# Kernel tuning notes

Measured on AMD Instinct MI355X. Metric: run time of the kernel, lower is better.

Reference implementation:

```python
import jax, jax.numpy as jnp
import numpy as np

SPATIAL_DIM = 2
N_IN = 4096
N_OUT = 1024
C_IN = 32
C_OUT = 32
FILTER_SEQ = (64, 64)
BATCH = 16


def _grid(num_points):
    # replicates: meshgrid(indexing='xy') of linspace(0,1,n) per dim, dstack, view(-1, d)
    n = int(num_points ** (1.0 / SPATIAL_DIM))
    nodes = np.linspace(0.0, 1.0, n)
    X, Y = np.meshgrid(nodes, nodes, indexing='xy')
    return np.dstack((X, Y)).reshape(-1, SPATIAL_DIM)  # (n^2, 2)


def _cache():
    # replicates QuadConvLayer.cache(): bump-support sparsity pattern
    out_locs = _grid(N_OUT)               # (N_OUT, 2)
    in_nodes = _grid(N_IN)                # (N_IN, 2)
    locs = out_locs[:, None, :] - in_nodes[None, :, :]   # (N_OUT, N_IN, 2)
    bump_arg = np.linalg.norm(locs, axis=2) ** 4
    decay_param = (N_IN / 16.0) ** 2
    mask = bump_arg <= 1.0 / decay_param
    idx = np.argwhere(mask)               # (E, 2), row-major sorted like torch.nonzero
    eval_locs = locs[mask]                # (E, 2)
    return eval_locs.astype(np.float32), idx.astype(np.int64)


def setup_inputs() -> dict:
    key = jax.random.key(0)
    k_feat, k1, k2, k3 = jax.random.split(key, 4)
    eval_locs, eval_indices = _cache()
    # filter MLP G: Linear(2,64,bias=False) -> Sin -> Linear(64,64) -> Sin -> Linear(64, C_IN*C_OUT)
    d0, d1, d2, d3 = SPATIAL_DIM, FILTER_SEQ[0], FILTER_SEQ[1], C_IN * C_OUT
    W1 = jax.random.normal(k1, (d0, d1), jnp.float32) / np.sqrt(d0)
    W2 = jax.random.normal(k2, (d1, d2), jnp.float32) / np.sqrt(d1)
    W3 = jax.random.normal(k3, (d2, d3), jnp.float32) / np.sqrt(d2)
    features = jax.random.normal(k_feat, (BATCH, C_IN, N_IN), jnp.float32)
    return {
        "features": features,
        "W1": W1,
        "W2": W2,
        "W3": W3,
        "eval_locs": jnp.asarray(eval_locs),
        "eval_indices": jnp.asarray(eval_indices),
    }


def reference(features, W1, W2, W3, eval_locs, eval_indices):
    B = features.shape[0]
    E = eval_locs.shape[0]
    seg = eval_indices[:, 0]   # output point per edge (sorted)
    src = eval_indices[:, 1]   # input point per edge
    # filter MLP with Sin activations: (E, 2) -> (E, C_IN, C_OUT)
    h = jnp.sin(eval_locs @ W1)
    h = jnp.sin(h @ W2)
    filt = (h @ W3).reshape(E, C_IN, C_OUT)
    # gather features at source points: (B, C_IN, E)
    gathered = features[:, :, src]
    # faithful to torch: a raw reshape (NOT a transpose) of (B, C_IN, E) -> (B, E, C_IN)
    g = gathered.reshape(B, E, C_IN)
    vals = jnp.einsum('bni,nij->bnj', g, filt)   # (B, E, C_OUT)
    # faithful raw reshape (B, E, C_OUT) -> (B, C_OUT, E)
    vals = vals.reshape(B, C_OUT, E)
    # scatter-sum over edges into output points (segment_coo sum)
    integral = jnp.zeros((B, C_OUT, N_OUT), features.dtype).at[:, :, seg].add(vals)
    return integral
```

## Files before the change

### kernel.cpp

```cpp
#include <hip/hip_runtime.h>
#include <hip/hip_bf16.h>

typedef __bf16 bf16x4  __attribute__((ext_vector_type(4)));
typedef __bf16 bf16x8  __attribute__((ext_vector_type(8)));
typedef __bf16 bf16x16 __attribute__((ext_vector_type(16)));
typedef float  f32x4   __attribute__((ext_vector_type(4)));

#define N_IN   4096
#define N_OUT  1024
#define BATCH  16
#define ROWS   16

#define H1_STR   72
#define H2_STR   72
#define FT_JSTR  40
#define FTH_NSTR 648
#define G_STR    520
#define V_STR    520
#define GSTR2    1048
#define VSTR2    1288
#define FB_FT_NSTR 1288
#define SEG_STR  34

#define WS_W3T_OFF    0
#define WS_W2T_OFF    131072
#define WS_FEATT_OFF  139264
#define WS_NEED       4333568

__global__ void qc_zero_kernel(float* __restrict__ out, int n4) {
    int i = blockIdx.x * blockDim.x + threadIdx.x;
    if (i < n4) ((float4*)out)[i] = make_float4(0.f, 0.f, 0.f, 0.f);
}

__global__ void qc_prep_kernel(const float* __restrict__ w3, const float* __restrict__ w2,
                               __bf16* __restrict__ w3t, __bf16* __restrict__ w2t) {
    int gid = blockIdx.x * blockDim.x + threadIdx.x;
    if (gid < 65536) {
        int k = gid & 63, col = gid >> 6;
        w3t[gid] = (__bf16)w3[k * 1024 + col];
    } else {
        int j = gid - 65536;
        int k = j & 63, col = j >> 6;
        w2t[j] = (__bf16)w2[k * 64 + col];
    }
}

__global__ void qc_prep2_kernel(const float* __restrict__ w3, const float* __restrict__ w2,
                                const float* __restrict__ feat,
                                float* __restrict__ out,
                                __bf16* __restrict__ w3t, __bf16* __restrict__ w2t,
                                __bf16* __restrict__ featT) {
    int bid = blockIdx.x, tid = threadIdx.x;
    if (bid < 512) {
        int c    = bid >> 4;
        int src  = (bid & 15) * 256 + tid;
        bf16x16 v;
        #pragma unroll
        for (int b = 0; b < 16; ++b)
            v[b] = (__bf16)feat[(b * 32 + c) * N_IN + src];
        __bf16* p = &featT[((size_t)c * N_IN + src) * 16];
        *(bf16x8*)p       = *(bf16x8*)&v;
        *(bf16x8*)(p + 8) = *((bf16x8*)&v + 1);
    } else if (bid < 528) {
        __shared__ float tile[64][65];
        const int colbase = (bid - 512) * 64;
        #pragma unroll
        for (int it = 0; it < 16; ++it) {
            int k = it * 4 + (tid >> 6);
            int c = tid & 63;
            tile[k][c] = w3[k * 1024 + colbase + c];
        }
        __syncthreads();
        int cc = tid >> 2;
        int k0 = (tid & 3) * 16;
        bf16x8 o0, o1;
        #pragma unroll
        for (int z = 0; z < 8; ++z) {
            o0[z] = (__bf16)tile[k0 + z][cc];
            o1[z] = (__bf16)tile[k0 + 8 + z][cc];
        }
        __bf16* wp = &w3t[(colbase + cc) * 64 + k0];
        *(bf16x8*)wp       = o0;
        *(bf16x8*)(wp + 8) = o1;
    } else if (bid == 528) {
        #pragma unroll
        for (int z = 0; z < 16; ++z) {
            int j = tid * 16 + z;
            w2t[j] = (__bf16)w2[(j & 63) * 64 + (j >> 6)];
        }
    } else {
        int i = (bid - 529) * 256 + tid;
        ((float4*)out)[i] = make_float4(0.f, 0.f, 0.f, 0.f);
    }
}

__global__ __launch_bounds__(512, 2)
void qc_fused32_kernel(const __bf16* __restrict__ featT,
                       const float* __restrict__ w1,
                       const float* __restrict__ locs,
                       const int*   __restrict__ eidx,
                       const __bf16* __restrict__ w2t,
                       const __bf16* __restrict__ w3t,
                       float* __restrict__ out,
                       int E)
{
    __shared__ __align__(16) unsigned char region1[41472];
    __shared__ __align__(16) __bf16 h1b[32 * H1_STR];
    __shared__ __align__(16) __bf16 h2b[32 * H2_STR];
    __shared__ unsigned short seg_s[32 * SEG_STR];

    __bf16* gb   = (__bf16*)region1;
    __bf16* ftv  = (__bf16*)region1;
    __bf16* vals = (__bf16*)region1;

    const int tid  = threadIdx.x;
    const int lane = tid & 63;
    const int wv   = tid >> 6;
    const int ml   = lane & 15;
    const int q    = lane >> 4;
    const int n0   = blockIdx.x * 32;
    const int t0   = n0 * 32;
    const int ch0  = t0 / E;
    const int m0   = t0 - ch0 * E;

    const int tlb = wv * 128 + lane;
    bf16x16 gvv[2];
    int sgv[2];
    #pragma unroll
    for (int h = 0; h < 2; ++h) {
        int tl = tlb + h * 64;
        int mm = m0 + tl;
        int cc = ch0 + (mm >= E);
        if (mm >= E) mm -= E;
        int2 p = ((const int2*)eidx)[mm];
        sgv[h] = p.x;
        int ccc = cc < 32 ? cc : 31;
        bf16x16 g = *(const bf16x16*)&featT[((size_t)ccc * N_IN + p.y) * 16];
        if (cc >= 32) {
            #pragma unroll
            for (int z = 0; z < 16; ++z) g[z] = (__bf16)0.f;
        }
        gvv[h] = g;
    }
    const int rg = (wv >> 2) * 16;
    const int cw = (wv & 3) * 16;
    const bf16x8 bw0 = *(const bf16x8*)&w2t[(cw + ml) * 64 + q * 8];
    const bf16x8 bw1 = *(const bf16x8*)&w2t[(cw + ml) * 64 + 32 + q * 8];

    {
        const int r  = tid >> 4;
        const int j0 = (tid & 15) * 4;
        float lx = 0.f, ly = 0.f;
        int n = n0 + r;
        if (n < E) { lx = locs[n * 2]; ly = locs[n * 2 + 1]; }
        float4 wa = *(const float4*)&w1[j0];
        float4 wb = *(const float4*)&w1[64 + j0];
        __bf16* hp = &h1b[r * H1_STR + j0];
        hp[0] = (__bf16)__sinf(lx * wa.x + ly * wb.x);
        hp[1] = (__bf16)__sinf(lx * wa.y + ly * wb.y);
        hp[2] = (__bf16)__sinf(lx * wa.z + ly * wb.z);
        hp[3] = (__bf16)__sinf(lx * wa.w + ly * wb.w);
    }
    __syncthreads();

    {
        bf16x8 a0 = *(const bf16x8*)&h1b[(rg + ml) * H1_STR + q * 8];
        bf16x8 a1 = *(const bf16x8*)&h1b[(rg + ml) * H1_STR + 32 + q * 8];
        f32x4 c = {0.f, 0.f, 0.f, 0.f};
        c = __builtin_amdgcn_mfma_f32_16x16x32_bf16(a0, bw0, c, 0, 0, 0);
        c = __builtin_amdgcn_mfma_f32_16x16x32_bf16(a1, bw1, c, 0, 0, 0);
        #pragma unroll
        for (int g_ = 0; g_ < 4; ++g_)
            h2b[(rg + q * 4 + g_) * H2_STR + cw + ml] = (__bf16)__sinf(c[g_]);
    }

    #pragma unroll
    for (int b = 0; b < 16; ++b) {
        gb[b * GSTR2 + tlb]      = gvv[0][b];
        gb[b * GSTR2 + tlb + 64] = gvv[1][b];
    }
    seg_s[(tlb >> 5) * SEG_STR + (tlb & 31)] = (unsigned short)sgv[0];
    {
        int tl1 = tlb + 64;
        seg_s[(tl1 >> 5) * SEG_STR + (tl1 & 31)] = (unsigned short)sgv[1];
    }
    bf16x8 ag[4];
    #pragma unroll
    for (int rr = 0; rr < 4; ++rr)
        ag[rr] = *(const bf16x8*)&gb[ml * GSTR2 + (wv * 4 + rr) * 32 + q * 8];
    __syncthreads();

    bf16x8 ha00 = *(const bf16x8*)&h2b[ml * H2_STR + q * 8];
    bf16x8 ha01 = *(const bf16x8*)&h2b[ml * H2_STR + 32 + q * 8];
    bf16x8 ha10 = *(const bf16x8*)&h2b[(16 + ml) * H2_STR + q * 8];
    bf16x8 ha11 = *(const bf16x8*)&h2b[(16 + ml) * H2_STR + 32 + q * 8];

    f32x4 c0[4], c1[4];

    {
        f32x4 accA[4], accB[4];
        #pragma unroll
        for (int tt = 0; tt < 4; ++tt) {
            int i_  = wv * 4 + tt;
            int col = i_ * 32 + ml;
            const __bf16* wp = &w3t[col * 64 + q * 8];
            bf16x8 b0 = *(const bf16x8*)wp;
            bf16x8 b1 = *(const bf16x8*)(wp + 32);
            f32x4 cA = {0.f, 0.f, 0.f, 0.f};
            f32x4 cB = {0.f, 0.f, 0.f, 0.f};
            cA = __builtin_amdgcn_mfma_f32_16x16x32_bf16(ha00, b0, cA, 0, 0, 0);
            cA = __builtin_amdgcn_mfma_f32_16x16x32_bf16(ha01, b1, cA, 0, 0, 0);
            cB = __builtin_amdgcn_mfma_f32_16x16x32_bf16(ha10, b0, cB, 0, 0, 0);
            cB = __builtin_amdgcn_mfma_f32_16x16x32_bf16(ha11, b1, cB, 0, 0, 0);
            accA[tt] = cA; accB[tt] = cB;
        }
        #pragma unroll
        for (int g_ = 0; g_ < 4; ++g_) {
            bf16x4 pa, pb;
            #pragma unroll
            for (int tt = 0; tt < 4; ++tt) {
                pa[tt] = (__bf16)accA[tt][g_];
                pb[tt] = (__bf16)accB[tt][g_];
            }
            *(bf16x4*)&ftv[(q * 4 + g_) * FTH_NSTR + ml * FT_JSTR + wv * 4]        = pa;
            *(bf16x4*)&ftv[(16 + q * 4 + g_) * FTH_NSTR + ml * FT_JSTR + wv * 4]   = pb;
        }
    }
    __syncthreads();

    {
        bf16x8 f[4];
        #pragma unroll
        for (int rr = 0; rr < 4; ++rr)
            f[rr] = *(const bf16x8*)&ftv[(wv * 4 + rr) * FTH_NSTR + ml * FT_JSTR + q * 8];
        #pragma unroll
        for (int rr = 0; rr < 4; ++rr) {
            f32x4 z = {0.f, 0.f, 0.f, 0.f};
            c0[rr] = __builtin_amdgcn_mfma_f32_16x16x32_bf16(ag[rr], f[rr], z, 0, 0, 0);
        }
    }
    __syncthreads();

    {
        f32x4 accA[4], accB[4];
        #pragma unroll
        for (int tt = 0; tt < 4; ++tt) {
            int i_  = wv * 4 + tt;
            int col = i_ * 32 + 16 + ml;
            const __bf16* wp = &w3t[col * 64 + q * 8];
            bf16x8 b0 = *(const bf16x8*)wp;
            bf16x8 b1 = *(const bf16x8*)(wp + 32);
            f32x4 cA = {0.f, 0.f, 0.f, 0.f};
            f32x4 cB = {0.f, 0.f, 0.f, 0.f};
            cA = __builtin_amdgcn_mfma_f32_16x16x32_bf16(ha00, b0, cA, 0, 0, 0);
            cA = __builtin_amdgcn_mfma_f32_16x16x32_bf16(ha01, b1, cA, 0, 0, 0);
            cB = __builtin_amdgcn_mfma_f32_16x16x32_bf16(ha10, b0, cB, 0, 0, 0);
            cB = __builtin_amdgcn_mfma_f32_16x16x32_bf16(ha11, b1, cB, 0, 0, 0);
            accA[tt] = cA; accB[tt] = cB;
        }
        #pragma unroll
        for (int g_ = 0; g_ < 4; ++g_) {
            bf16x4 pa, pb;
            #pragma unroll
            for (int tt = 0; tt < 4; ++tt) {
                pa[tt] = (__bf16)accA[tt][g_];
                pb[tt] = (__bf16)accB[tt][g_];
            }
            *(bf16x4*)&ftv[(q * 4 + g_) * FTH_NSTR + ml * FT_JSTR + wv * 4]        = pa;
            *(bf16x4*)&ftv[(16 + q * 4 + g_) * FTH_NSTR + ml * FT_JSTR + wv * 4]   = pb;
        }
    }
    __syncthreads();

    bf16x8 f1[4];
    #pragma unroll
    for (int rr = 0; rr < 4; ++rr)
        f1[rr] = *(const bf16x8*)&ftv[(wv * 4 + rr) * FTH_NSTR + ml * FT_JSTR + q * 8];
    __syncthreads();
    #pragma unroll
    for (int rr = 0; rr < 4; ++rr) {
        f32x4 z = {0.f, 0.f, 0.f, 0.f};
        c1[rr] = __builtin_amdgcn_mfma_f32_16x16x32_bf16(ag[rr], f1[rr], z, 0, 0, 0);
    }
    #pragma unroll
    for (int rr = 0; rr < 4; ++rr) {
        int r = wv * 4 + rr;
        __bf16* vp = &vals[r * FT_JSTR];
        #pragma unroll
        for (int g_ = 0; g_ < 4; ++g_) {
            int b = q * 4 + g_;
            vp[b * VSTR2 + ml]      = (__bf16)c0[rr][g_];
            vp[b * VSTR2 + 16 + ml] = (__bf16)c1[rr][g_];
        }
    }
    __syncthreads();

    {
        const int be = tid >> 5;
        const int w  = tid & 31;
        const __bf16* vp = &vals[be * VSTR2 + w * FT_JSTR];
        bf16x8 v0 = *(const bf16x8*)(vp);
        bf16x8 v1 = *(const bf16x8*)(vp + 8);
        bf16x8 v2 = *(const bf16x8*)(vp + 16);
        bf16x8 v3 = *(const bf16x8*)(vp + 24);
        float vv[32];
        #pragma unroll
        for (int j = 0; j < 8; ++j) {
            vv[j]      = (float)v0[j];
            vv[8 + j]  = (float)v1[j];
            vv[16 + j] = (float)v2[j];
            vv[24 + j] = (float)v3[j];
        }
        int mwin = m0 + (w << 5);
        int cb   = ch0;
        if (mwin >= E) { mwin -= E; ++cb; }
        int jcross = E - mwin;
        int base0 = (cb < 32)     ? ((be << 15) | (cb << 10))       : -1;
        int base1 = (cb + 1 < 32) ? ((be << 15) | ((cb + 1) << 10)) : -1;
        int key_prev = -1;
        float acc = 0.f;
        #pragma unroll
        for (int j = 0; j < 32; ++j) {
            int basej = (j < jcross) ? base0 : base1;
            if (basej >= 0) {
                int key = basej + (int)seg_s[w * SEG_STR + j];
                if (key != key_prev) {
                    if (key_prev >= 0) atomicAdd(&out[key_prev], acc);
                    key_prev = key;
                    acc = vv[j];
                } else {
                    acc += vv[j];
                }
            }
        }
        if (key_prev >= 0) atomicAdd(&out[key_prev], acc);
    }
}

__global__ __launch_bounds__(256, 2)
void qc_main_kernel(const float* __restrict__ feat,
                    const float* __restrict__ w1,
                    const float* __restrict__ w2,
                    const float* __restrict__ locs,
                    const int*   __restrict__ eidx,
                    const __bf16* __restrict__ w3t,
                    float* __restrict__ out,
                    int E)
{
    __shared__ __align__(16) __bf16 h1b[ROWS * H1_STR];
    __shared__ __align__(16) __bf16 h2b[ROWS * H2_STR];
    __shared__ __align__(16) __bf16 ftv[ROWS * FB_FT_NSTR];
    __shared__ __align__(16) __bf16 gb [BATCH * G_STR];
    __shared__ unsigned short seg_s[512];
    __shared__ unsigned short src_s[512];

    const int tid = threadIdx.x;
    const int n0  = blockIdx.x * ROWS;
    const int t0  = n0 * 32;
    const int ch0 = t0 / E;
    const int m0  = t0 - ch0 * E;

    {
        const int r  = tid >> 4;
        const int j0 = (tid & 15) * 4;
        float lx = 0.f, ly = 0.f;
        int n = n0 + r;
        if (n < E) { lx = locs[n * 2]; ly = locs[n * 2 + 1]; }
        float4 wa = *(const float4*)&w1[j0];
        float4 wb = *(const float4*)&w1[64 + j0];
        __bf16* h = &h1b[r * H1_STR + j0];
        h[0] = (__bf16)__sinf(lx * wa.x + ly * wb.x);
        h[1] = (__bf16)__sinf(lx * wa.y + ly * wb.y);
        h[2] = (__bf16)__sinf(lx * wa.z + ly * wb.z);
        h[3] = (__bf16)__sinf(lx * wa.w + ly * wb.w);
    }
    for (int tl = tid; tl < 512; tl += 256) {
        int mm = m0 + tl; if (mm >= E) mm -= E;
        seg_s[tl] = (unsigned short)eidx[mm * 2];
        src_s[tl] = (unsigned short)eidx[mm * 2 + 1];
    }
    __syncthreads();

    {
        const int r  = tid >> 4;
        const int j0 = (tid & 15) * 4;
        float a0 = 0.f, a1 = 0.f, a2 = 0.f, a3 = 0.f;
        const __bf16* h1r = &h1b[r * H1_STR];
        #pragma unroll 8
        for (int k = 0; k < 64; ++k) {
            float h = (float)h1r[k];
            float4 w = *(const float4*)&w2[k * 64 + j0];
            a0 += h * w.x; a1 += h * w.y; a2 += h * w.z; a3 += h * w.w;
        }
        __bf16* h = &h2b[r * H2_STR + j0];
        h[0] = (__bf16)__sinf(a0);
        h[1] = (__bf16)__sinf(a1);
        h[2] = (__bf16)__sinf(a2);
        h[3] = (__bf16)__sinf(a3);
    }
    #pragma unroll 4
    for (int it = 0; it < 32; ++it) {
        int idx = it * 256 + tid;
        int b   = idx >> 9;
        int tl  = idx & 511;
        int mm  = m0 + tl;
        int cc  = ch0 + (mm >= E);
        if (mm >= E) mm -= E;
        float v = 0.f;
        if (cc < 32) v = feat[(b * 32 + cc) * N_IN + (int)src_s[tl]];
        gb[b * G_STR + tl] = (__bf16)v;
    }
    __syncthreads();

    const int lane = tid & 63;
    const int wv   = tid >> 6;
    const int ml   = lane & 15;
    const int q    = lane >> 4;

    {
        bf16x8 a0 = *(const bf16x8*)&h2b[ml * H2_STR + q * 8];
        bf16x8 a1 = *(const bf16x8*)&h2b[ml * H2_STR + 32 + q * 8];
        #pragma unroll
        for (int t = 0; t < 16; ++t) {
            int col = wv * 256 + t * 16 + ml;
            const __bf16* wp = &w3t[col * 64 + q * 8];
            bf16x8 b0 = *(const bf16x8*)wp;
            bf16x8 b1 = *(const bf16x8*)(wp + 32);
            f32x4 c = {0.f, 0.f, 0.f, 0.f};
            c = __builtin_amdgcn_mfma_f32_16x16x32_bf16(a0, b0, c, 0, 0, 0);
            c = __builtin_amdgcn_mfma_f32_16x16x32_bf16(a1, b1, c, 0, 0, 0);
            int i_ = col >> 5, j_ = col & 31;
            __bf16* fp = &ftv[j_ * FT_JSTR + i_];
            fp[(q * 4 + 0) * FB_FT_NSTR] = (__bf16)c[0];
            fp[(q * 4 + 1) * FB_FT_NSTR] = (__bf16)c[1];
            fp[(q * 4 + 2) * FB_FT_NSTR] = (__bf16)c[2];
            fp[(q * 4 + 3) * FB_FT_NSTR] = (__bf16)c[3];
        }
    }
    __syncthreads();

    {
        bf16x8 ag[4], f0[4], f1[4];
        #pragma unroll
        for (int rr = 0; rr < 4; ++rr) {
            int r = wv * 4 + rr;
            ag[rr] = *(const bf16x8*)&gb[ml * G_STR + r * 32 + q * 8];
            f0[rr] = *(const bf16x8*)&ftv[r * FB_FT_NSTR + ml        * FT_JSTR + q * 8];
            f1[rr] = *(const bf16x8*)&ftv[r * FB_FT_NSTR + (16 + ml) * FT_JSTR + q * 8];
        }
        __syncthreads();
        __bf16* valsb = ftv;
        #pragma unroll
        for (int rr = 0; rr < 4; ++rr) {
            int r = wv * 4 + rr;
            f32x4 c0 = {0.f, 0.f, 0.f, 0.f};
            f32x4 c1 = {0.f, 0.f, 0.f, 0.f};
            c0 = __builtin_amdgcn_mfma_f32_16x16x32_bf16(ag[rr], f0[rr], c0, 0, 0, 0);
            c1 = __builtin_amdgcn_mfma_f32_16x16x32_bf16(ag[rr], f1[rr], c1, 0, 0, 0);
            __bf16* vp = &valsb[r * 32];
            #pragma unroll
            for (int g_ = 0; g_ < 4; ++g_) {
                int b = q * 4 + g_;
                vp[b * V_STR + ml]      = (__bf16)c0[g_];
                vp[b * V_STR + 16 + ml] = (__bf16)c1[g_];
            }
        }
    }
    __syncthreads();

    {
        const __bf16* valsb = ftv;
        const int b = tid >> 4;
        const int r = tid & 15;
        const __bf16* vp = &valsb[b * V_STR + r * 32];
        bf16x8 v0 = *(const bf16x8*)(vp);
        bf16x8 v1 = *(const bf16x8*)(vp + 8);
        bf16x8 v2 = *(const bf16x8*)(vp + 16);
        bf16x8 v3 = *(const bf16x8*)(vp + 24);
        float vv[32];
        #pragma unroll
        for (int j = 0; j < 8; ++j) {
            vv[j]      = (float)v0[j];
            vv[8 + j]  = (float)v1[j];
            vv[16 + j] = (float)v2[j];
            vv[24 + j] = (float)v3[j];
        }
        const int tl0 = r * 32;
        int key_prev = -1;
        float acc = 0.f;
        #pragma unroll
        for (int j = 0; j < 32; ++j) {
            int mm = m0 + tl0 + j;
            int cc = ch0 + (mm >= E);
            if (mm >= E) mm -= E;
            if (cc < 32) {
                int o   = (int)seg_s[tl0 + j];
                int key = ((b * 32 + cc) << 10) | o;
                if (key != key_prev) {
                    if (key_prev >= 0) atomicAdd(&out[key_prev], acc);
                    key_prev = key;
                    acc = vv[j];
                } else {
                    acc += vv[j];
                }
            }
        }
        if (key_prev >= 0) atomicAdd(&out[key_prev], acc);
    }
}

extern "C" void kernel_launch(void* const* d_in, const int* in_sizes, int n_in,
                              void* d_out, int out_size, void* d_ws, size_t ws_size,
                              hipStream_t stream)
{
    (void)n_in;
    const float* feat = (const float*)d_in[0];
    const float* w1   = (const float*)d_in[1];
    const float* w2   = (const float*)d_in[2];
    const float* w3   = (const float*)d_in[3];
    const float* locs = (const float*)d_in[4];
    const int*   eidx = (const int*)d_in[5];
    float* out  = (float*)d_out;

    const int E = in_sizes[4] / 2;
    if (E <= 0) return;

    __bf16* w3t   = (__bf16*)((char*)d_ws + WS_W3T_OFF);
    __bf16* w2t   = (__bf16*)((char*)d_ws + WS_W2T_OFF);
    __bf16* featT = (__bf16*)((char*)d_ws + WS_FEATT_OFF);

    if (ws_size >= (size_t)WS_NEED) {
        int nblocks = (E + 31) / 32;
        qc_prep2_kernel<<<1041, 256, 0, stream>>>(w3, w2, feat, out, w3t, w2t, featT);
        qc_fused32_kernel<<<nblocks, 512, 0, stream>>>(featT, w1, locs, eidx, w2t, w3t, out, E);
    } else {
        int n4 = out_size / 4;
        int nblocks = (E + ROWS - 1) / ROWS;
        qc_zero_kernel<<<(n4 + 255) / 256, 256, 0, stream>>>(out, n4);
        qc_prep_kernel<<<272, 256, 0, stream>>>(w3, w2, w3t, w2t);
        qc_main_kernel<<<nblocks, 256, 0, stream>>>(feat, w1, w2, locs, eidx, w3t, out, E);
    }
}
```

Measured before the change: 134.2 us.

## Stage segment-sum scatter in shared-memory tile before writing to global output

The per-edge scatter now accumulates into a per-block shared-memory tile indexed by output segment, instead of issuing global atomics directly. After a barrier, interior segments are written with plain stores and only boundary segments, which may be shared with neighbouring blocks, use global atomics. This reuses the MLP LDS region for the tile and keeps the old global-atomic path as a fallback when the segment span exceeds the tile size. It adds LDS zeroing, an extra barrier and a serial loop over batches in exchange for fewer contended global atomics.

Measured after the change: 127.3 us. 5.2% less time.

```diff
diff --git a/kernel.cpp b/kernel.cpp
--- a/kernel.cpp
+++ b/kernel.cpp
@@ -21,6 +21,7 @@
 #define VSTR2    1288
 #define FB_FT_NSTR 1288
 #define SEG_STR  34
+#define TILE_K   144
 
 #define WS_W3T_OFF    0
 #define WS_W2T_OFF    131072
@@ -105,13 +106,16 @@
                        int E)
 {
     __shared__ __align__(16) unsigned char region1[41472];
-    __shared__ __align__(16) __bf16 h1b[32 * H1_STR];
-    __shared__ __align__(16) __bf16 h2b[32 * H2_STR];
+    __shared__ __align__(16) unsigned char region2[9216];
     __shared__ unsigned short seg_s[32 * SEG_STR];
 
     __bf16* gb   = (__bf16*)region1;
     __bf16* ftv  = (__bf16*)region1;
     __bf16* vals = (__bf16*)region1;
+
+    __bf16* h1b  = (__bf16*)region2;
+    __bf16* h2b  = (__bf16*)(region2 + 9216/2);
+    float*  tile = (float*)region2;
 
     const int tid  = threadIdx.x;
     const int lane = tid & 63;
@@ -228,6 +232,12 @@
     }
     __syncthreads();
 
+    #pragma unroll
+    for (int z = 0; z < 5; ++z) {
+        int i = tid + z * 512;
+        if (i < 16 * TILE_K) tile[i] = 0.f;
+    }
+
     {
         bf16x8 f[4];
         #pragma unroll
@@ -311,29 +321,85 @@
             vv[16 + j] = (float)v2[j];
             vv[24 + j] = (float)v3[j];
         }
+
+        const int seg0 = (int)seg_s[0];
+        const int segL = (int)seg_s[31 * SEG_STR + 31];
+        const int tlw  = E - m0;
+        const bool wrap = (tlw < 1024);
+        int OFF = 0, NK;
+        if (wrap) {
+            int tw = tlw - 1;
+            OFF = (int)seg_s[(tw >> 5) * SEG_STR + (tw & 31)] - seg0 + 1;
+            NK  = OFF + segL + 1;
+        } else {
+            NK = segL - seg0 + 1;
+        }
+
         int mwin = m0 + (w << 5);
         int cb   = ch0;
         if (mwin >= E) { mwin -= E; ++cb; }
         int jcross = E - mwin;
-        int base0 = (cb < 32)     ? ((be << 15) | (cb << 10))       : -1;
-        int base1 = (cb + 1 < 32) ? ((be << 15) | ((cb + 1) << 10)) : -1;
-        int key_prev = -1;
-        float acc = 0.f;
-        #pragma unroll
-        for (int j = 0; j < 32; ++j) {
-            int basej = (j < jcross) ? base0 : base1;
-            if (basej >= 0) {
-                int key = basej + (int)seg_s[w * SEG_STR + j];
-                if (key != key_prev) {
-                    if (key_prev >= 0) atomicAdd(&out[key_prev], acc);
-                    key_prev = key;
-                    acc = vv[j];
-                } else {
-                    acc += vv[j];
+
+        if (NK <= TILE_K) {
+            const int NEG = -0x40000000;
+            int io0 = (cb < 32) ? ((cb == ch0) ? -seg0 : OFF) : NEG;
+            int io1 = (cb + 1 < 32) ? OFF : NEG;
+            int key_prev = -1;
+            float acc = 0.f;
+            #pragma unroll
+            for (int j = 0; j < 32; ++j) {
+                int io = (j < jcross) ? io0 : io1;
+                if (io != NEG) {
+                    int key = io + (int)seg_s[w * SEG_STR + j];
+                    if (key != key_prev) {
+                        if (key_prev >= 0) atomicAdd(&tile[be * TILE_K + key_prev], acc);
+                        key_prev = key;
+                        acc = vv[j];
+                    } else {
+                        acc += vv[j];
+                    }
                 }
             }
-        }
-        if (key_prev >= 0) atomicAdd(&out[key_prev], acc);
+            if (key_prev >= 0) atomicAdd(&tile[be * TILE_K + key_prev], acc);
+
+            __syncthreads();
+
+            for (int bb = 0; bb < 16; ++bb) {
+                for (int i = tid; i < NK; i += 512) {
+                    int cbx, sg;
+                    if (wrap && i >= OFF) { cbx = ch0 + 1; sg = i - OFF; }
+                    else                  { cbx = ch0;     sg = seg0 + i; }
+                    if (cbx < 32) {
+                        float v = tile[bb * TILE_K + i];
+                        int o = (bb << 15) | (cbx << 10) | sg;
+                        bool bnd = (i == 0) || (i == NK - 1) ||
+                                   (wrap && (i == OFF - 1 || i == OFF));
+                        if (bnd) atomicAdd(&out[o], v);
+                        else     out[o] = v;
+                    }
+                }
+            }
+        } else {
+            int base0 = (cb < 32)     ? ((be << 15) | (cb << 10))       : -1;
+            int base1 = (cb + 1 < 32) ? ((be << 15) | ((cb + 1) << 10)) : -1;
+            int key_prev = -1;
+            float acc = 0.f;
+            #pragma unroll
+            for (int j = 0; j < 32; ++j) {
+                int basej = (j < jcross) ? base0 : base1;
+                if (basej >= 0) {
+                    int key = basej + (int)seg_s[w * SEG_STR + j];
+                    if (key != key_prev) {
+                        if (key_prev >= 0) atomicAdd(&out[key_prev], acc);
+                        key_prev = key;
+                        acc = vv[j];
+                    } else {
+                        acc += vv[j];
+                    }
+                }
+            }
+            if (key_prev >= 0) atomicAdd(&out[key_prev], acc);
+        }
     }
 }
 
```
